# Performance work log

Hardware: AMD Instinct MI355X
Metric: run time of the kernel (lower is better)

Reference implementation:

```python
import jax, jax.numpy as jnp
import numpy as np


def setup_inputs() -> dict:
    key = jax.random.key(0)
    k1, k2, k3, k4 = jax.random.split(key, 4)
    n, C, t, h, w = 1, 256, 8, 64, 64
    heads = 8
    S = t + h + w - 2  # 134 axial positions per query
    attention = jax.random.normal(k1, (n, heads * S, t, h, w), dtype=jnp.float32)
    value = jax.random.normal(k2, (n, C, t, h, w), dtype=jnp.float32)
    conv_w = jax.random.normal(k3, (C, C), dtype=jnp.float32) / np.float32(np.sqrt(C))
    conv_b = jax.random.normal(k4, (C,), dtype=jnp.float32)
    return {"attention": attention, "value": value, "conv_w": conv_w,
            "conv_b": conv_b, "num_heads": heads}


def _grid_attn_map(A, V):
    """Criss-cross axial attention aggregation.
    A: [b, t+h+w-2, t, h, w] per-query weights over the t-axis (t entries,
       self included), h-axis (h-1 entries, self excluded) and w-axis
       (w-1 entries, self excluded).
    V: [b, c, t, h, w]. Returns [b, c, t, h, w].
    """
    b, c, t, h, w = V.shape
    A_t = A[:, :t]                  # [b, t, t, h, w]
    A_h = A[:, t:t + h - 1]         # [b, h-1, t, h, w]
    A_w = A[:, t + h - 1:]          # [b, w-1, t, h, w]

    # t-axis (self included): sum over key frame s
    out = jnp.einsum('bsthw,bcshw->bcthw', A_t, V)

    # h-axis (self excluded): channel j addresses key row p = j + (j >= q).
    # Build dense [h] channel axis with a zero at p == q via a padded gather.
    zpad = jnp.zeros((b, 1, t, h, w), A.dtype)
    A_h_pad = jnp.concatenate([A_h, zpad], axis=1)  # channel h-1 is zero
    p = jnp.arange(h)[:, None]
    q = jnp.arange(h)[None, :]
    inv_h = jnp.where(p < q, p, jnp.where(p == q, h - 1, p - 1))  # [h(p), h(q)]
    A_h_full = jnp.take_along_axis(A_h_pad, inv_h[None, :, None, :, None], axis=1)  # [b,p,t,q,w]
    out = out + jnp.einsum('bptqw,bctpw->bctqw', A_h_full, V)

    # w-axis (self excluded), same trick along w
    A_w_pad = jnp.concatenate([A_w, zpad], axis=1)  # channel w-1 is zero (h==w here OK; recompute pad generally)
    pw = jnp.arange(w)[:, None]
    qw = jnp.arange(w)[None, :]
    inv_w = jnp.where(pw < qw, pw, jnp.where(pw == qw, w - 1, pw - 1))  # [w(p), w(q)]
    A_w_full = jnp.take_along_axis(A_w_pad, inv_w[None, :, None, None, :], axis=1)  # [b,p,t,h,q]
    out = out + jnp.einsum('bpthq,bcthp->bcthq', A_w_full, V)
    return out


def reference(attention, value, conv_w, conv_b, num_heads):
    n, C, t, h, w = value.shape
    S = t + h + w - 2
    # 1x1x1 Conv3d == per-position channel matmul
    pv = jnp.einsum('ncthw,oc->nothw', value, conv_w) + conv_b[None, :, None, None, None]
    pv = pv.reshape(n * num_heads, C // num_heads, t, h, w)
    A = attention.reshape(n * num_heads, S, t, h, w)
    out = _grid_attn_map(A, pv)
    return out.reshape(n, num_heads, C // num_heads, t, h, w)
```

## Files before the change

kernel.cpp:

```cpp
#include <hip/hip_runtime.h>

#define SS   134
#define HWP  4096
#define THW  32768

typedef float f32x4 __attribute__((ext_vector_type(4)));
typedef short bf16x8 __attribute__((ext_vector_type(8)));
typedef short bf16x4 __attribute__((ext_vector_type(4)));

__device__ __forceinline__ unsigned short f2bf(float f) {
  unsigned int u = __float_as_uint(f);
  u += 0x7fff + ((u >> 16) & 1);
  return (unsigned short)(u >> 16);
}

__global__ __launch_bounds__(256) void w2bf(const float* __restrict__ W,
                                            unsigned short* __restrict__ Wbf) {
  const int i = (blockIdx.x * 256 + threadIdx.x) * 4;
  const float4 w4 = *(const float4*)&W[i];
  bf16x4 b;
  b.x = (short)f2bf(w4.x);
  b.y = (short)f2bf(w4.y);
  b.z = (short)f2bf(w4.z);
  b.w = (short)f2bf(w4.w);
  *(bf16x4*)&Wbf[i] = b;
}

__global__ __launch_bounds__(256) void conv1x1_v3(
    const float* __restrict__ V, const unsigned short* __restrict__ Wbf,
    const float* __restrict__ bias, float* __restrict__ PV) {
  __shared__ unsigned short sW[256 * 40];
  __shared__ unsigned short sV[32 * 40];
  const int tid = threadIdx.x;
  const int x0 = blockIdx.x * 32;
  const int lane = tid & 63;
  const int wv = tid >> 6;
  const int m = lane & 15;
  const int q = lane >> 4;

  f32x4 acc[4][2];
#pragma unroll
  for (int i = 0; i < 4; ++i)
#pragma unroll
    for (int j = 0; j < 2; ++j)
      acc[i][j] = (f32x4){0.f, 0.f, 0.f, 0.f};

  for (int k0 = 0; k0 < 256; k0 += 32) {
#pragma unroll
    for (int r = 0; r < 4; ++r) {
      const int s8 = r * 256 + tid;
      const int o = s8 >> 2;
      const int c8 = (s8 & 3) * 8;
      *(bf16x8*)&sW[o * 40 + c8] = *(const bf16x8*)&Wbf[o * 256 + k0 + c8];
    }
    {
      const int c = tid >> 3;
      const int x4 = (tid & 7) * 4;
      const float4 v4 = *(const float4*)&V[(size_t)(k0 + c) * THW + x0 + x4];
      sV[(x4 + 0) * 40 + c] = f2bf(v4.x);
      sV[(x4 + 1) * 40 + c] = f2bf(v4.y);
      sV[(x4 + 2) * 40 + c] = f2bf(v4.z);
      sV[(x4 + 3) * 40 + c] = f2bf(v4.w);
    }
    __syncthreads();
    bf16x8 fa[4], fb[2];
#pragma unroll
    for (int i = 0; i < 4; ++i)
      fa[i] = *(const bf16x8*)&sW[(wv * 64 + i * 16 + m) * 40 + q * 8];
#pragma unroll
    for (int j = 0; j < 2; ++j)
      fb[j] = *(const bf16x8*)&sV[(j * 16 + m) * 40 + q * 8];
#pragma unroll
    for (int i = 0; i < 4; ++i)
#pragma unroll
      for (int j = 0; j < 2; ++j)
        acc[i][j] = __builtin_amdgcn_mfma_f32_16x16x32_bf16(fa[i], fb[j], acc[i][j], 0, 0, 0);
    __syncthreads();
  }

#pragma unroll
  for (int i = 0; i < 4; ++i) {
#pragma unroll
    for (int r = 0; r < 4; ++r) {
      const int o = wv * 64 + i * 16 + q * 4 + r;
      const float b = bias[o];
#pragma unroll
      for (int j = 0; j < 2; ++j)
        PV[(size_t)o * THW + x0 + j * 16 + m] = acc[i][j][r] + b;
    }
  }
}

__global__ __launch_bounds__(256) void attn_t(
    const float* __restrict__ A, const float* __restrict__ PV,
    float* __restrict__ O) {
  const int b = blockIdx.x;
  const int hd = b & 7;
  const int cb = (b >> 3) & 3;
  const int xt = b >> 5;
  const int tid = threadIdx.x;
  const int xi = xt * 256 + (tid & 63) * 4;
  const int cq = tid >> 6;

  const float* __restrict__ At = A + (size_t)hd * SS * THW + xi;
  const size_t pvh = (size_t)hd * 32 * THW;

  f32x4 acc[8][2];
#pragma unroll
  for (int t = 0; t < 8; ++t)
#pragma unroll
    for (int ci = 0; ci < 2; ++ci)
      acc[t][ci] = (f32x4){0.f, 0.f, 0.f, 0.f};

  for (int s = 0; s < 8; ++s) {
    f32x4 pvv[2];
#pragma unroll
    for (int ci = 0; ci < 2; ++ci) {
      const int c = cb * 8 + cq * 2 + ci;
      pvv[ci] = *(const f32x4*)&PV[pvh + (size_t)c * THW + (size_t)s * HWP + xi];
    }
#pragma unroll
    for (int t = 0; t < 8; ++t) {
      const f32x4 a = *(const f32x4*)&At[(size_t)s * THW + (size_t)t * HWP];
#pragma unroll
      for (int ci = 0; ci < 2; ++ci)
        acc[t][ci] += a * pvv[ci];
    }
  }

#pragma unroll
  for (int t = 0; t < 8; ++t)
#pragma unroll
    for (int ci = 0; ci < 2; ++ci) {
      const int c = cb * 8 + cq * 2 + ci;
      *(f32x4*)&O[pvh + (size_t)c * THW + (size_t)t * HWP + xi] = acc[t][ci];
    }
}

__global__ __launch_bounds__(512) void attn_h(
    const float* __restrict__ A, const float* __restrict__ PV,
    float* __restrict__ O) {
  const int b = blockIdx.x;
  const int hd = b & 7;
  const int qb = (b >> 3) & 3;
  const int tq = b >> 5;
  const int tid = threadIdx.x;
  const int lane = tid & 63;
  const int wv = tid >> 6;
  const int w4 = (lane & 15) * 4;
  const int cl = lane >> 4;
  const int ch = wv & 1;
  const int qg = wv >> 1;
  const int q0 = qb * 16 + qg * 4;

  __shared__ float slab[2][8 * 32 * 64];

  const float* __restrict__ Ab = A + (size_t)hd * SS * THW + (size_t)tq * HWP;
  const size_t pvh = (size_t)hd * 32 * THW;
  const float* __restrict__ PVh = PV + pvh;

  f32x4 acc[4][4];
#pragma unroll
  for (int qi = 0; qi < 4; ++qi) {
    const int q = q0 + qi;
#pragma unroll
    for (int g = 0; g < 4; ++g) {
      const int c = ch * 16 + g * 4 + cl;
      acc[qi][g] =
          *(const f32x4*)&O[pvh + (size_t)c * THW + (size_t)tq * HWP + q * 64 + w4];
    }
  }

  const int c_s = tid >> 4;
  const int w4s = (tid & 15) * 4;
  const float* __restrict__ pvstage =
      PVh + (size_t)c_s * THW + (size_t)tq * HWP + w4s;
  const int sbase = c_s * 64 + w4s;

  f32x4 stg[8];
#pragma unroll
  for (int r = 0; r < 8; ++r) stg[r] = *(const f32x4*)&pvstage[r * 64];
#pragma unroll
  for (int r = 0; r < 8; ++r)
    *(f32x4*)&slab[0][r * 2048 + sbase] = stg[r];
  __syncthreads();

  for (int ck = 0; ck < 8; ++ck) {
    const int cur = ck & 1;
    if (ck < 7) {
#pragma unroll
      for (int r = 0; r < 8; ++r)
        stg[r] = *(const f32x4*)&pvstage[((ck + 1) * 8 + r) * 64];
    }
#pragma unroll
    for (int pp = 0; pp < 8; ++pp) {
      const int p = ck * 8 + pp;
      f32x4 a[4];
#pragma unroll
      for (int qi = 0; qi < 4; ++qi) {
        const int q = q0 + qi;
        const int row = p - (q < p ? 1 : 0);
        f32x4 av = *(const f32x4*)&Ab[(size_t)(8 + row) * THW + q * 64 + w4];
        if (q == p) av = (f32x4){0.f, 0.f, 0.f, 0.f};
        a[qi] = av;
      }
      f32x4 v[4];
#pragma unroll
      for (int g = 0; g < 4; ++g)
        v[g] = *(const f32x4*)&slab[cur][pp * 2048 + (g * 4 + cl + ch * 16) * 64 + w4];
#pragma unroll
      for (int qi = 0; qi < 4; ++qi)
#pragma unroll
        for (int g = 0; g < 4; ++g)
          acc[qi][g] += a[qi] * v[g];
    }
    __syncthreads();
    if (ck < 7) {
#pragma unroll
      for (int r = 0; r < 8; ++r)
        *(f32x4*)&slab[cur ^ 1][r * 2048 + sbase] = stg[r];
      __syncthreads();
    }
  }

#pragma unroll
  for (int qi = 0; qi < 4; ++qi) {
    const int q = q0 + qi;
#pragma unroll
    for (int g = 0; g < 4; ++g) {
      const int c = ch * 16 + g * 4 + cl;
      *(f32x4*)&O[pvh + (size_t)c * THW + (size_t)tq * HWP + q * 64 + w4] =
          acc[qi][g];
    }
  }
}

__global__ __launch_bounds__(256) void attn_w(
    const float* __restrict__ A, const float* __restrict__ PV,
    float* __restrict__ O) {
  const int b = blockIdx.x;
  const int hb = b & 15;
  const int tq = (b >> 4) & 7;
  const int hd = b >> 7;
  const int tid = threadIdx.x;
  const int wq = tid & 63;
  const int cg = tid >> 6;
  const int h0 = hb * 4;

  __shared__ float slab[32 * 64 * 4];

  const float* __restrict__ Ab = A + (size_t)hd * SS * THW + (size_t)tq * HWP;
  const size_t pvh = (size_t)hd * 32 * THW;

#pragma unroll 4
  for (int i = 0; i < 8; ++i) {
    const int fid = tid + i * 256;
    const int w4s = (fid & 15) * 4;
    const int h = (fid >> 4) & 3;
    const int c = fid >> 6;
    const f32x4 v =
        *(const f32x4*)&PV[pvh + (size_t)c * THW + (size_t)tq * HWP + (h0 + h) * 64 + w4s];
    slab[(c * 64 + w4s + 0) * 4 + h] = v.x;
    slab[(c * 64 + w4s + 1) * 4 + h] = v.y;
    slab[(c * 64 + w4s + 2) * 4 + h] = v.z;
    slab[(c * 64 + w4s + 3) * 4 + h] = v.w;
  }

  f32x4 racc[8];
#pragma unroll
  for (int ci = 0; ci < 8; ++ci) {
    const int c = cg + ci * 4;
    f32x4 r;
#pragma unroll
    for (int hh = 0; hh < 4; ++hh)
      r[hh] = O[pvh + (size_t)c * THW + (size_t)tq * HWP + (h0 + hh) * 64 + wq];
    racc[ci] = r;
  }
  __syncthreads();

#pragma unroll 2
  for (int p = 0; p < 64; ++p) {
    const int row = 71 + p - (wq <= p ? 1 : 0);
    const float* pa = Ab + (size_t)row * THW + h0 * 64 + wq;
    f32x4 a;
    a.x = pa[0];
    a.y = pa[64];
    a.z = pa[128];
    a.w = pa[192];
    if (p == wq) a = (f32x4){0.f, 0.f, 0.f, 0.f};
#pragma unroll
    for (int ci = 0; ci < 8; ++ci) {
      const f32x4 v = *(const f32x4*)&slab[(cg + ci * 4) * 256 + p * 4];
      racc[ci] += a * v;
    }
  }

#pragma unroll
  for (int ci = 0; ci < 8; ++ci) {
    const int c = cg + ci * 4;
#pragma unroll
    for (int hh = 0; hh < 4; ++hh)
      O[pvh + (size_t)c * THW + (size_t)tq * HWP + (h0 + hh) * 64 + wq] = racc[ci][hh];
  }
}

extern "C" void kernel_launch(void* const* d_in, const int* in_sizes, int n_in,
                              void* d_out, int out_size, void* d_ws, size_t ws_size,
                              hipStream_t stream) {
  const float* A = (const float*)d_in[0];
  const float* V = (const float*)d_in[1];
  const float* W = (const float*)d_in[2];
  const float* bias = (const float*)d_in[3];
  float* out = (float*)d_out;
  float* pv = (float*)d_ws;

  unsigned short* Wbf = (unsigned short*)d_out;

  w2bf<<<dim3(64), 256, 0, stream>>>(W, Wbf);
  conv1x1_v3<<<dim3(1024), 256, 0, stream>>>(V, Wbf, bias, pv);
  attn_t<<<dim3(512), 256, 0, stream>>>(A, pv, out);
  attn_h<<<dim3(256), 512, 0, stream>>>(A, pv, out);
  attn_w<<<dim3(1024), 256, 0, stream>>>(A, pv, out);
}
```

Measured before the change: 370.4 us.

## Restructure conv tiling with resident weights, shrink attn_h slab, unroll attn_w

The conv kernel now loads the whole bf16 weight matrix into LDS once per block, processes 128 positions per block with 512 threads, and double-buffers the V tiles so the next chunk's global loads overlap the MFMAs. This removes the per-k-step reloading of weights and halves the number of barriers per step. attn_h halves its LDS slab (chunks of 4 rows instead of 8) and folds the staging store before a single barrier, which should raise occupancy. attn_w's inner loop unroll goes from 2 to 4. The large LDS weight buffer (~133KB) limits conv occupancy to one block per CU.

```diff
diff --git a/kernel.cpp b/kernel.cpp
--- a/kernel.cpp
+++ b/kernel.cpp
@@ -26,67 +26,94 @@
   *(bf16x4*)&Wbf[i] = b;
 }
 
-__global__ __launch_bounds__(256) void conv1x1_v3(
+__global__ __launch_bounds__(512) void conv1x1_v4(
     const float* __restrict__ V, const unsigned short* __restrict__ Wbf,
     const float* __restrict__ bias, float* __restrict__ PV) {
-  __shared__ unsigned short sW[256 * 40];
-  __shared__ unsigned short sV[32 * 40];
+  __shared__ unsigned short sW[256 * 260];
+  __shared__ unsigned short sV[2][128 * 40];
   const int tid = threadIdx.x;
-  const int x0 = blockIdx.x * 32;
+  const int x0 = blockIdx.x * 128;
   const int lane = tid & 63;
   const int wv = tid >> 6;
   const int m = lane & 15;
   const int q = lane >> 4;
 
-  f32x4 acc[4][2];
-#pragma unroll
-  for (int i = 0; i < 4; ++i)
-#pragma unroll
-    for (int j = 0; j < 2; ++j)
+  {
+    const int o = tid >> 1;
+    const int half = (tid & 1) * 128;
+#pragma unroll
+    for (int r = 0; r < 16; ++r)
+      *(bf16x8*)&sW[o * 260 + half + r * 8] =
+          *(const bf16x8*)&Wbf[o * 256 + half + r * 8];
+  }
+
+  const int c_s = tid >> 4;
+  const int x8 = (tid & 15) * 8;
+  const float* __restrict__ vstage = V + (size_t)c_s * THW + x0 + x8;
+
+  {
+    const float4 va = *(const float4*)&vstage[0];
+    const float4 vb = *(const float4*)&vstage[4];
+    sV[0][(x8 + 0) * 40 + c_s] = f2bf(va.x);
+    sV[0][(x8 + 1) * 40 + c_s] = f2bf(va.y);
+    sV[0][(x8 + 2) * 40 + c_s] = f2bf(va.z);
+    sV[0][(x8 + 3) * 40 + c_s] = f2bf(va.w);
+    sV[0][(x8 + 4) * 40 + c_s] = f2bf(vb.x);
+    sV[0][(x8 + 5) * 40 + c_s] = f2bf(vb.y);
+    sV[0][(x8 + 6) * 40 + c_s] = f2bf(vb.z);
+    sV[0][(x8 + 7) * 40 + c_s] = f2bf(vb.w);
+  }
+  __syncthreads();
+
+  f32x4 acc[2][8];
+#pragma unroll
+  for (int i = 0; i < 2; ++i)
+#pragma unroll
+    for (int j = 0; j < 8; ++j)
       acc[i][j] = (f32x4){0.f, 0.f, 0.f, 0.f};
 
-  for (int k0 = 0; k0 < 256; k0 += 32) {
+  for (int kk = 0; kk < 8; ++kk) {
+    const int cur = kk & 1;
+    float4 pva, pvb;
+    if (kk < 7) {
+      pva = *(const float4*)&vstage[(size_t)(kk + 1) * 32 * THW];
+      pvb = *(const float4*)&vstage[(size_t)(kk + 1) * 32 * THW + 4];
+    }
+    bf16x8 fa[2], fb[8];
+#pragma unroll
+    for (int i = 0; i < 2; ++i)
+      fa[i] = *(const bf16x8*)&sW[(wv * 32 + i * 16 + m) * 260 + kk * 32 + q * 8];
+#pragma unroll
+    for (int j = 0; j < 8; ++j)
+      fb[j] = *(const bf16x8*)&sV[cur][(j * 16 + m) * 40 + q * 8];
+#pragma unroll
+    for (int i = 0; i < 2; ++i)
+#pragma unroll
+      for (int j = 0; j < 8; ++j)
+        acc[i][j] = __builtin_amdgcn_mfma_f32_16x16x32_bf16(fa[i], fb[j], acc[i][j], 0, 0, 0);
+    if (kk < 7) {
+      const int nb = cur ^ 1;
+      sV[nb][(x8 + 0) * 40 + c_s] = f2bf(pva.x);
+      sV[nb][(x8 + 1) * 40 + c_s] = f2bf(pva.y);
+      sV[nb][(x8 + 2) * 40 + c_s] = f2bf(pva.z);
+      sV[nb][(x8 + 3) * 40 + c_s] = f2bf(pva.w);
+      sV[nb][(x8 + 4) * 40 + c_s] = f2bf(pvb.x);
+      sV[nb][(x8 + 5) * 40 + c_s] = f2bf(pvb.y);
+      sV[nb][(x8 + 6) * 40 + c_s] = f2bf(pvb.z);
+      sV[nb][(x8 + 7) * 40 + c_s] = f2bf(pvb.w);
+    }
+    __syncthreads();
+  }
+
+#pragma unroll
+  for (int i = 0; i < 2; ++i) {
 #pragma unroll
     for (int r = 0; r < 4; ++r) {
-      const int s8 = r * 256 + tid;
-      const int o = s8 >> 2;
-      const int c8 = (s8 & 3) * 8;
-      *(bf16x8*)&sW[o * 40 + c8] = *(const bf16x8*)&Wbf[o * 256 + k0 + c8];
-    }
-    {
-      const int c = tid >> 3;
-      const int x4 = (tid & 7) * 4;
-      const float4 v4 = *(const float4*)&V[(size_t)(k0 + c) * THW + x0 + x4];
-      sV[(x4 + 0) * 40 + c] = f2bf(v4.x);
-      sV[(x4 + 1) * 40 + c] = f2bf(v4.y);
-      sV[(x4 + 2) * 40 + c] = f2bf(v4.z);
-      sV[(x4 + 3) * 40 + c] = f2bf(v4.w);
-    }
-    __syncthreads();
-    bf16x8 fa[4], fb[2];
-#pragma unroll
-    for (int i = 0; i < 4; ++i)
-      fa[i] = *(const bf16x8*)&sW[(wv * 64 + i * 16 + m) * 40 + q * 8];
-#pragma unroll
-    for (int j = 0; j < 2; ++j)
-      fb[j] = *(const bf16x8*)&sV[(j * 16 + m) * 40 + q * 8];
-#pragma unroll
-    for (int i = 0; i < 4; ++i)
-#pragma unroll
-      for (int j = 0; j < 2; ++j)
-        acc[i][j] = __builtin_amdgcn_mfma_f32_16x16x32_bf16(fa[i], fb[j], acc[i][j], 0, 0, 0);
-    __syncthreads();
-  }
-
-#pragma unroll
-  for (int i = 0; i < 4; ++i) {
-#pragma unroll
-    for (int r = 0; r < 4; ++r) {
-      const int o = wv * 64 + i * 16 + q * 4 + r;
-      const float b = bias[o];
-#pragma unroll
-      for (int j = 0; j < 2; ++j)
-        PV[(size_t)o * THW + x0 + j * 16 + m] = acc[i][j][r] + b;
+      const int o = wv * 32 + i * 16 + q * 4 + r;
+      const float bo = bias[o];
+#pragma unroll
+      for (int j = 0; j < 8; ++j)
+        PV[(size_t)o * THW + x0 + j * 16 + m] = acc[i][j][r] + bo;
     }
   }
 }
@@ -153,7 +180,7 @@
   const int qg = wv >> 1;
   const int q0 = qb * 16 + qg * 4;
 
-  __shared__ float slab[2][8 * 32 * 64];
+  __shared__ float slab[2][4 * 32 * 64];
 
   const float* __restrict__ Ab = A + (size_t)hd * SS * THW + (size_t)tq * HWP;
   const size_t pvh = (size_t)hd * 32 * THW;
@@ -177,24 +204,24 @@
       PVh + (size_t)c_s * THW + (size_t)tq * HWP + w4s;
   const int sbase = c_s * 64 + w4s;
 
-  f32x4 stg[8];
-#pragma unroll
-  for (int r = 0; r < 8; ++r) stg[r] = *(const f32x4*)&pvstage[r * 64];
-#pragma unroll
-  for (int r = 0; r < 8; ++r)
+  f32x4 stg[4];
+#pragma unroll
+  for (int r = 0; r < 4; ++r) stg[r] = *(const f32x4*)&pvstage[r * 64];
+#pragma unroll
+  for (int r = 0; r < 4; ++r)
     *(f32x4*)&slab[0][r * 2048 + sbase] = stg[r];
   __syncthreads();
 
-  for (int ck = 0; ck < 8; ++ck) {
+  for (int ck = 0; ck < 16; ++ck) {
     const int cur = ck & 1;
-    if (ck < 7) {
-#pragma unroll
-      for (int r = 0; r < 8; ++r)
-        stg[r] = *(const f32x4*)&pvstage[((ck + 1) * 8 + r) * 64];
-    }
-#pragma unroll
-    for (int pp = 0; pp < 8; ++pp) {
-      const int p = ck * 8 + pp;
+    if (ck < 15) {
+#pragma unroll
+      for (int r = 0; r < 4; ++r)
+        stg[r] = *(const f32x4*)&pvstage[((ck + 1) * 4 + r) * 64];
+    }
+#pragma unroll
+    for (int pp = 0; pp < 4; ++pp) {
+      const int p = ck * 4 + pp;
       f32x4 a[4];
 #pragma unroll
       for (int qi = 0; qi < 4; ++qi) {
@@ -214,13 +241,12 @@
         for (int g = 0; g < 4; ++g)
           acc[qi][g] += a[qi] * v[g];
     }
+    if (ck < 15) {
+#pragma unroll
+      for (int r = 0; r < 4; ++r)
+        *(f32x4*)&slab[cur ^ 1][r * 2048 + sbase] = stg[r];
+    }
     __syncthreads();
-    if (ck < 7) {
-#pragma unroll
-      for (int r = 0; r < 8; ++r)
-        *(f32x4*)&slab[cur ^ 1][r * 2048 + sbase] = stg[r];
-      __syncthreads();
-    }
   }
 
 #pragma unroll
@@ -278,7 +304,7 @@
   }
   __syncthreads();
 
-#pragma unroll 2
+#pragma unroll 4
   for (int p = 0; p < 64; ++p) {
     const int row = 71 + p - (wq <= p ? 1 : 0);
     const float* pa = Ab + (size_t)row * THW + h0 * 64 + wq;
@@ -317,7 +343,7 @@
   unsigned short* Wbf = (unsigned short*)d_out;
 
   w2bf<<<dim3(64), 256, 0, stream>>>(W, Wbf);
-  conv1x1_v3<<<dim3(1024), 256, 0, stream>>>(V, Wbf, bias, pv);
+  conv1x1_v4<<<dim3(256), 512, 0, stream>>>(V, Wbf, bias, pv);
   attn_t<<<dim3(512), 256, 0, stream>>>(A, pv, out);
   attn_h<<<dim3(256), 512, 0, stream>>>(A, pv, out);
   attn_w<<<dim3(1024), 256, 0, stream>>>(A, pv, out);
```

New measurement: 353.3 us. 4.6% less time.
